# Optimization experiments

Hardware: AMD Instinct MI355X
Metric: run time of the kernel (lower is better)

The kernel has to match this reference:

```python
import jax, jax.numpy as jnp
import numpy as np

EPS = 1e-5

def setup_inputs() -> dict:
    key = jax.random.key(0)
    k1, k2 = jax.random.split(key)
    x = jax.random.normal(k1, (32, 256, 56, 56), dtype=jnp.float32)
    conv_w = jax.random.normal(k2, (1, 2, 5, 5), dtype=jnp.float32) * 0.1
    gamma = jnp.ones((1,), dtype=jnp.float32)
    beta = jnp.zeros((1,), dtype=jnp.float32)
    return {"x": x, "conv_w": conv_w, "gamma": gamma, "beta": beta}

def reference(x, conv_w, gamma, beta):
    # channel max and mean -> [N, 2, H, W]
    y = jnp.stack([jnp.max(x, axis=1), jnp.mean(x, axis=1)], axis=1)
    # 5x5 conv, 2->1 channels, SAME padding, no bias -> [N, 1, H, W]
    y = jax.lax.conv_general_dilated(
        y, conv_w, window_strides=(1, 1), padding=((2, 2), (2, 2)),
        dimension_numbers=("NCHW", "OIHW", "NCHW"))
    # BatchNorm2d(1) in training mode: batch statistics over (N, H, W)
    mean = jnp.mean(y, axis=(0, 2, 3), keepdims=True)
    var = jnp.mean(jnp.square(y - mean), axis=(0, 2, 3), keepdims=True)
    y = (y - mean) * jax.lax.rsqrt(var + EPS)
    y = y * gamma.reshape(1, -1, 1, 1) + beta.reshape(1, -1, 1, 1)
    # double sigmoid gate, broadcast over channels
    return x * jax.nn.sigmoid(jax.nn.sigmoid(y))
```

## Files before the change

### kernel.cpp

```cpp
#include <hip/hip_runtime.h>

#define NN 32
#define CC 256
#define HH 56
#define WW 56
#define HWSZ 3136
#define QPP 784
#define NQ 25088
#define NHW 100352
#define CBLKS 32
#define APPLY_THREADS (NQ * CBLKS)

typedef float v4f __attribute__((ext_vector_type(4)));

__device__ __forceinline__ float4 f4max(float4 a, float4 b) {
    float4 r;
    r.x = fmaxf(a.x, b.x); r.y = fmaxf(a.y, b.y);
    r.z = fmaxf(a.z, b.z); r.w = fmaxf(a.w, b.w);
    return r;
}
__device__ __forceinline__ float4 f4add(float4 a, float4 b) {
    float4 r;
    r.x = a.x + b.x; r.y = a.y + b.y; r.z = a.z + b.z; r.w = a.w + b.w;
    return r;
}

__global__ __launch_bounds__(512) void k_pool(const float* __restrict__ x,
                                              float* __restrict__ pool,
                                              float* __restrict__ stats) {
    if (blockIdx.x == 0 && threadIdx.x == 0 && threadIdx.y == 0) {
        stats[0] = 0.f;
        stats[1] = 0.f;
    }
    const int tx = threadIdx.x;
    const int ty = threadIdx.y;
    const int qid = blockIdx.x * 64 + tx;
    const int n = qid / QPP;
    const int hwq = qid - n * QPP;

    const float4* p = (const float4*)x + (size_t)(n * CC + ty * 32) * QPP + hwq;
    float4 v0 = p[0];
    float4 vmax = v0, vsum = v0;
#pragma unroll 8
    for (int i = 1; i < 32; ++i) {
        float4 v = p[(size_t)i * QPP];
        vmax = f4max(vmax, v);
        vsum = f4add(vsum, v);
    }
    __shared__ float4 smax[8][64];
    __shared__ float4 ssum[8][64];
    smax[ty][tx] = vmax;
    ssum[ty][tx] = vsum;
    __syncthreads();
    if (ty == 0) {
        float4 m = smax[0][tx];
        float4 s = ssum[0][tx];
#pragma unroll
        for (int g = 1; g < 8; ++g) {
            m = f4max(m, smax[g][tx]);
            s = f4add(s, ssum[g][tx]);
        }
        float4* pm = (float4*)pool + (size_t)n * 2 * QPP + hwq;
        pm[0] = m;
        float4 mean;
        mean.x = s.x * 0.00390625f; mean.y = s.y * 0.00390625f;
        mean.z = s.z * 0.00390625f; mean.w = s.w * 0.00390625f;
        pm[QPP] = mean;
    }
}

__global__ __launch_bounds__(256) void k_conv(const float* __restrict__ pool,
                                              const float* __restrict__ cw,
                                              float* __restrict__ conv,
                                              float* __restrict__ stats) {
    __shared__ float w[50];
    const int tid = threadIdx.x;
    if (tid < 50) w[tid] = cw[tid];
    __syncthreads();

    const int gid = blockIdx.x * 256 + tid;
    const int n = gid / HWSZ;
    const int hw = gid - n * HWSZ;
    const int h = hw / WW;
    const int wc = hw - h * WW;

    const float* pb = pool + (size_t)n * 2 * HWSZ;
    float acc = 0.f;
#pragma unroll
    for (int ci = 0; ci < 2; ++ci)
#pragma unroll
        for (int kh = 0; kh < 5; ++kh) {
            const int hh = h + kh - 2;
            if (hh < 0 || hh >= HH) continue;
#pragma unroll
            for (int kw = 0; kw < 5; ++kw) {
                const int wwc = wc + kw - 2;
                if (wwc < 0 || wwc >= WW) continue;
                acc += pb[ci * HWSZ + hh * WW + wwc] * w[ci * 25 + kh * 5 + kw];
            }
        }
    conv[gid] = acc;

    float s = acc, s2 = acc * acc;
#pragma unroll
    for (int i = 1; i < 64; i <<= 1) {
        s += __shfl_xor(s, i);
        s2 += __shfl_xor(s2, i);
    }
    if ((tid & 63) == 0) {
        atomicAdd(&stats[0], s);
        atomicAdd(&stats[1], s2);
    }
}

__global__ __launch_bounds__(256) void k_apply(const float* __restrict__ x,
                                               const float* __restrict__ conv,
                                               const float* __restrict__ stats,
                                               const float* __restrict__ gamma,
                                               const float* __restrict__ beta,
                                               float* __restrict__ out) {
    const float invM = 1.f / (float)NHW;
    const float mean = stats[0] * invM;
    const float var = stats[1] * invM - mean * mean;
    const float scale = rsqrtf(var + 1e-5f) * gamma[0];
    const float shift = beta[0] - mean * scale;

    const int gid = blockIdx.x * 256 + threadIdx.x;
    const int v = gid / QPP;
    const int hwq = gid - v * QPP;
    const int cblk = v & (CBLKS - 1);
    const int n = v >> 5;

    const float4 cv = ((const float4*)conv)[n * QPP + hwq];
    float4 g;
    {
        float t = cv.x * scale + shift;
        float s1 = 1.f / (1.f + __expf(-t));
        g.x = 1.f / (1.f + __expf(-s1));
    }
    {
        float t = cv.y * scale + shift;
        float s1 = 1.f / (1.f + __expf(-t));
        g.y = 1.f / (1.f + __expf(-s1));
    }
    {
        float t = cv.z * scale + shift;
        float s1 = 1.f / (1.f + __expf(-t));
        g.z = 1.f / (1.f + __expf(-s1));
    }
    {
        float t = cv.w * scale + shift;
        float s1 = 1.f / (1.f + __expf(-t));
        g.w = 1.f / (1.f + __expf(-s1));
    }

    const float4* x4 = (const float4*)x + (size_t)(n * CC + cblk * 8) * QPP + hwq;
    v4f* o4 = (v4f*)out + (size_t)(n * CC + cblk * 8) * QPP + hwq;
#pragma unroll
    for (int i = 0; i < 8; ++i) {
        float4 xv = x4[(size_t)i * QPP];
        v4f r;
        r.x = xv.x * g.x; r.y = xv.y * g.y;
        r.z = xv.z * g.z; r.w = xv.w * g.w;
        __builtin_nontemporal_store(r, &o4[(size_t)i * QPP]);
    }
}

extern "C" void kernel_launch(void* const* d_in, const int* in_sizes, int n_in,
                              void* d_out, int out_size, void* d_ws, size_t ws_size,
                              hipStream_t stream) {
    const float* x = (const float*)d_in[0];
    const float* cw = (const float*)d_in[1];
    const float* gamma = (const float*)d_in[2];
    const float* beta = (const float*)d_in[3];
    float* out = (float*)d_out;

    float* ws = (float*)d_ws;
    float* pool = ws;
    float* conv = ws + 2 * NHW;
    float* stats = ws + 3 * NHW;

    k_pool<<<392, dim3(64, 8), 0, stream>>>(x, pool, stats);
    k_conv<<<392, 256, 0, stream>>>(pool, cw, conv, stats);
    k_apply<<<APPLY_THREADS / 256, 256, 0, stream>>>(x, conv, stats, gamma,
                                                     beta, out);
}
```

Before: 97.78 us.

## Split channel pooling across four blocks per tile with a separate merge kernel

The channel max/sum reduction is split so each spatial tile is handled by four blocks, each reducing a quarter of the channels into partial buffers. A new merge kernel combines the partials and writes the pooled max and mean. This raises the number of blocks reading the input to better saturate memory bandwidth, at the cost of an extra kernel launch and a small partial-result round trip through global memory.

Measured after the change: 100.6 us. +2.8%, slower.

```diff
diff --git a/kernel.cpp b/kernel.cpp
--- a/kernel.cpp
+++ b/kernel.cpp
@@ -25,30 +25,34 @@
     return r;
 }
 
-__global__ __launch_bounds__(512) void k_pool(const float* __restrict__ x,
-                                              float* __restrict__ pool,
-                                              float* __restrict__ stats) {
+__global__ __launch_bounds__(256) void k_pool_part(const float* __restrict__ x,
+                                                   float* __restrict__ pmaxp,
+                                                   float* __restrict__ psump,
+                                                   float* __restrict__ stats) {
     if (blockIdx.x == 0 && threadIdx.x == 0 && threadIdx.y == 0) {
         stats[0] = 0.f;
         stats[1] = 0.f;
     }
     const int tx = threadIdx.x;
     const int ty = threadIdx.y;
-    const int qid = blockIdx.x * 64 + tx;
+    const int tile = blockIdx.x >> 2;
+    const int quarter = blockIdx.x & 3;
+    const int qid = tile * 64 + tx;
     const int n = qid / QPP;
     const int hwq = qid - n * QPP;
-
-    const float4* p = (const float4*)x + (size_t)(n * CC + ty * 32) * QPP + hwq;
+    const int cbase = quarter * 64 + ty * 16;
+
+    const float4* p = (const float4*)x + (size_t)(n * CC + cbase) * QPP + hwq;
     float4 v0 = p[0];
     float4 vmax = v0, vsum = v0;
 #pragma unroll 8
-    for (int i = 1; i < 32; ++i) {
+    for (int i = 1; i < 16; ++i) {
         float4 v = p[(size_t)i * QPP];
         vmax = f4max(vmax, v);
         vsum = f4add(vsum, v);
     }
-    __shared__ float4 smax[8][64];
-    __shared__ float4 ssum[8][64];
+    __shared__ float4 smax[4][64];
+    __shared__ float4 ssum[4][64];
     smax[ty][tx] = vmax;
     ssum[ty][tx] = vsum;
     __syncthreads();
@@ -56,17 +60,34 @@
         float4 m = smax[0][tx];
         float4 s = ssum[0][tx];
 #pragma unroll
-        for (int g = 1; g < 8; ++g) {
+        for (int g = 1; g < 4; ++g) {
             m = f4max(m, smax[g][tx]);
             s = f4add(s, ssum[g][tx]);
         }
-        float4* pm = (float4*)pool + (size_t)n * 2 * QPP + hwq;
-        pm[0] = m;
-        float4 mean;
-        mean.x = s.x * 0.00390625f; mean.y = s.y * 0.00390625f;
-        mean.z = s.z * 0.00390625f; mean.w = s.w * 0.00390625f;
-        pm[QPP] = mean;
-    }
+        ((float4*)pmaxp)[(size_t)quarter * NQ + qid] = m;
+        ((float4*)psump)[(size_t)quarter * NQ + qid] = s;
+    }
+}
+
+__global__ __launch_bounds__(256) void k_merge(const float* __restrict__ pmaxp,
+                                               const float* __restrict__ psump,
+                                               float* __restrict__ pool) {
+    const int q = blockIdx.x * 256 + threadIdx.x;
+    if (q >= NQ) return;
+    float4 m = ((const float4*)pmaxp)[q];
+    float4 s = ((const float4*)psump)[q];
+#pragma unroll
+    for (int g = 1; g < 4; ++g) {
+        m = f4max(m, ((const float4*)pmaxp)[(size_t)g * NQ + q]);
+        s = f4add(s, ((const float4*)psump)[(size_t)g * NQ + q]);
+    }
+    const int n = q / QPP;
+    const int hwq = q - n * QPP;
+    ((float4*)pool)[(size_t)n * 2 * QPP + hwq] = m;
+    float4 mean;
+    mean.x = s.x * 0.00390625f; mean.y = s.y * 0.00390625f;
+    mean.z = s.z * 0.00390625f; mean.w = s.w * 0.00390625f;
+    ((float4*)pool)[(size_t)n * 2 * QPP + QPP + hwq] = mean;
 }
 
 __global__ __launch_bounds__(256) void k_conv(const float* __restrict__ pool,
@@ -176,11 +197,14 @@
     float* out = (float*)d_out;
 
     float* ws = (float*)d_ws;
-    float* pool = ws;
-    float* conv = ws + 2 * NHW;
-    float* stats = ws + 3 * NHW;
-
-    k_pool<<<392, dim3(64, 8), 0, stream>>>(x, pool, stats);
+    float* pmaxp = ws;
+    float* psump = pmaxp + (size_t)4 * NQ * 4;
+    float* pool = psump + (size_t)4 * NQ * 4;
+    float* conv = pool + 2 * NHW;
+    float* stats = conv + NHW;
+
+    k_pool_part<<<1568, dim3(64, 4), 0, stream>>>(x, pmaxp, psump, stats);
+    k_merge<<<98, 256, 0, stream>>>(pmaxp, psump, pool);
     k_conv<<<392, 256, 0, stream>>>(pool, cw, conv, stats);
     k_apply<<<APPLY_THREADS / 256, 256, 0, stream>>>(x, conv, stats, gamma,
                                                      beta, out);
```
